# Kernel tuning notes

Hardware: AMD Instinct MI355X
Metric: run time of the kernel (lower is better)

Reference implementation:

```python
import jax, jax.numpy as jnp
import numpy as np

NUM_HEADS = 16
NUM_KV_HEADS = 4
ROPE_BASE = 10000.0
TRAIN_SEQ_LEN = 1024


def _rms_norm(x):
    eps = jnp.finfo(x.dtype).eps
    var = jnp.mean(jnp.square(x), axis=-1, keepdims=True)
    return x * jax.lax.rsqrt(var + eps)


def _rotary_cos_sin(seq_len, head_dim, dtype):
    # NTK-by-parts base scaling when seq_len > train_seq_len (matches Rotary.forward)
    if seq_len > TRAIN_SEQ_LEN:
        scale = seq_len / TRAIN_SEQ_LEN
        base = ROPE_BASE * scale ** (head_dim / (head_dim - 2))
    else:
        base = ROPE_BASE
    inv_freq = 1.0 / base ** (jnp.arange(0, head_dim, 2, dtype=jnp.float32) / head_dim)
    t = jnp.arange(seq_len, dtype=jnp.float32)
    freqs = jnp.outer(t, inv_freq)  # [S, head_dim//2]
    return jnp.cos(freqs).astype(dtype), jnp.sin(freqs).astype(dtype)


def _apply_rotary(x, cos, sin):
    # x: [B,S,H,D]; cos/sin: [S, D//2] broadcast over batch and heads
    half = x.shape[-1] // 2
    x1, x2 = x[..., :half], x[..., half:]
    c = cos[None, :, None, :]
    s = sin[None, :, None, :]
    return jnp.concatenate((x1 * c + x2 * s, -x1 * s + x2 * c), axis=-1)


def setup_inputs() -> dict:
    key = jax.random.key(0)
    ks = jax.random.split(key, 5)
    B, S, D = 2, 2048, 2048
    KVD = NUM_KV_HEADS * (D // NUM_HEADS)
    x = jax.random.normal(ks[0], (B, S, D), dtype=jnp.float32)
    Wq = jax.random.normal(ks[1], (D, D), dtype=jnp.float32) * 0.02
    Wk = jax.random.normal(ks[2], (KVD, D), dtype=jnp.float32) * 0.02
    Wv = jax.random.normal(ks[3], (KVD, D), dtype=jnp.float32) * 0.02
    Wproj = jax.random.normal(ks[4], (D, D), dtype=jnp.float32) * 0.02
    q_gain = jnp.ones((NUM_HEADS,), dtype=jnp.float32)
    return {"x": x, "Wq": Wq, "Wk": Wk, "Wv": Wv, "Wproj": Wproj, "q_gain": q_gain}


def reference(x, Wq, Wk, Wv, Wproj, q_gain):
    B, S, D = x.shape
    H, KH = NUM_HEADS, NUM_KV_HEADS
    hd = D // H
    group = H // KH

    q = (x @ Wq.T).reshape(B, S, H, hd)
    k = (x @ Wk.T).reshape(B, S, KH, hd)
    v = (x @ Wv.T).reshape(B, S, KH, hd)

    q = _rms_norm(q)
    k = _rms_norm(k)

    cos, sin = _rotary_cos_sin(S, hd, q.dtype)
    q = _apply_rotary(q, cos, sin)
    k = _apply_rotary(k, cos, sin)

    q = q * q_gain.astype(q.dtype)[None, None, :, None]

    # GQA: query head h attends to kv head h // group
    k = jnp.repeat(k, group, axis=2)  # [B,S,H,hd]
    v = jnp.repeat(v, group, axis=2)

    scale = 1.0 / jnp.sqrt(jnp.asarray(hd, dtype=q.dtype))
    scores = jnp.einsum("bshd,bthd->bhst", q, k) * scale  # [B,H,S,S]
    causal = jnp.tril(jnp.ones((S, S), dtype=bool))
    scores = jnp.where(causal[None, None], scores, jnp.asarray(-jnp.inf, scores.dtype))
    probs = jax.nn.softmax(scores, axis=-1)
    out = jnp.einsum("bhst,bthd->bshd", probs, v)  # [B,S,H,hd]

    return out.reshape(B, S, D) @ Wproj.T
```

## Files before the change

### kernel.cpp

```cpp
#include <hip/hip_runtime.h>
#include <cmath>

typedef unsigned short u16;
typedef short v8s __attribute__((ext_vector_type(8)));
typedef float v4f __attribute__((ext_vector_type(4)));
typedef unsigned short v4u __attribute__((ext_vector_type(4)));
typedef unsigned int v2u __attribute__((ext_vector_type(2)));

__device__ __forceinline__ u16 f2bf(float f) {
  unsigned u = __builtin_bit_cast(unsigned, f);
  u += 0x7fffu + ((u >> 16) & 1u);
  return (u16)(u >> 16);
}
__device__ __forceinline__ float bf2f(u16 h) {
  unsigned u = ((unsigned)h) << 16;
  return __builtin_bit_cast(float, u);
}
__device__ __forceinline__ unsigned pk2(float a, float b) {
  return (unsigned)f2bf(a) | ((unsigned)f2bf(b) << 16);
}

__global__ void k_cast_bf16(const float* __restrict__ in, u16* __restrict__ out, int n4) {
  int i = blockIdx.x * blockDim.x + threadIdx.x;
  if (i >= n4) return;
  v4f v = ((const v4f*)in)[i];
  v4u o;
  o[0] = f2bf(v[0]); o[1] = f2bf(v[1]); o[2] = f2bf(v[2]); o[3] = f2bf(v[3]);
  ((v4u*)out)[i] = o;
}

__global__ void k_cast_w(const float* __restrict__ a, const float* __restrict__ b,
                         const float* __restrict__ c, const float* __restrict__ d,
                         u16* __restrict__ oa, u16* __restrict__ ob, u16* __restrict__ oc,
                         u16* __restrict__ od, int na4, int nb4, int nc4, int nd4) {
  int j = blockIdx.x * blockDim.x + threadIdx.x;
  const float* src;
  u16* dst;
  if (j < na4) { src = a; dst = oa; }
  else {
    j -= na4;
    if (j < nb4) { src = b; dst = ob; }
    else {
      j -= nb4;
      if (j < nc4) { src = c; dst = oc; }
      else {
        j -= nc4;
        if (j >= nd4) return;
        src = d; dst = od;
      }
    }
  }
  v4f v = ((const v4f*)src)[j];
  v4u o;
  o[0] = f2bf(v[0]); o[1] = f2bf(v[1]); o[2] = f2bf(v[2]); o[3] = f2bf(v[3]);
  ((v4u*)dst)[j] = o;
}

__global__ void k_rope_tab(float* __restrict__ cosT, float* __restrict__ sinT, float log2_base) {
  int idx = blockIdx.x * blockDim.x + threadIdx.x;
  int t = idx >> 6, i = idx & 63;
  float inv = exp2f(-(float)i * (1.0f / 64.0f) * log2_base);
  float fr = (float)t * inv;
  cosT[idx] = cosf(fr);
  sinT[idx] = sinf(fr);
}

__global__ void k_rmsnorm_rope(u16* __restrict__ qk, const float* __restrict__ cosT,
                               const float* __restrict__ sinT, const float* __restrict__ gain,
                               int H, int S, float oscale) {
  int row = blockIdx.x * 4 + (threadIdx.x >> 6);
  int l = threadIdx.x & 63;
  int h = row % H;
  int m = row / H;
  int s = m % S;
  u16* p = qk + (size_t)row * 128;
  float a = bf2f(p[l]), b = bf2f(p[64 + l]);
  float ss = a * a + b * b;
#pragma unroll
  for (int o = 32; o; o >>= 1) ss += __shfl_xor(ss, o, 64);
  float r = rsqrtf(ss * (1.0f / 128.0f) + 1.1920929e-7f);
  a *= r; b *= r;
  float c = cosT[s * 64 + l], sn = sinT[s * 64 + l];
  float o1 = a * c + b * sn;
  float o2 = b * c - a * sn;
  float g = oscale;
  if (gain != nullptr) g *= gain[h];
  p[l] = f2bf(o1 * g);
  p[64 + l] = f2bf(o2 * g);
}

__device__ __forceinline__ void stage8(char* sL, const u16* __restrict__ Ag,
                                       const u16* __restrict__ Bg, int row0, int col0, int K,
                                       int n, int NT2, int tid) {
  int tile = n >> 2;
  if (tile >= NT2) return;
  int part = n & 3;
  int isB = (part & 1);
  int half = (part == 1 || part == 2) ? 1 : 0;
  const u16* src0 = isB ? Bg : Ag;
  int g0 = (isB ? col0 : row0) + half * 128;
  int k0 = tile * 64;
  char* base = sL + ((tile & 1) * 65536 + isB * 32768 + half * 16384);
#pragma unroll
  for (int j = 0; j < 2; ++j) {
    int o = (j * 512 + tid) * 16;
    int rowp = o >> 8;
    int off = o & 255;
    int un = off ^ ((rowp & 15) << 4);
    int rsub = rowp + ((un >> 7) << 6);
    int k = (un & 127) >> 1;
    const u16* src = src0 + (size_t)(g0 + rsub) * K + (k0 + k);
    __builtin_amdgcn_global_load_lds((const __attribute__((address_space(1))) void*)src,
                                     (__attribute__((address_space(3))) void*)(base + o), 16, 0, 0);
  }
}

#define PH(BUF, MH, NH, LA, LB, WAITC)                                                            \
  {                                                                                               \
    if (LA) {                                                                                     \
      _Pragma("unroll") for (int mi = 0; mi < 4; ++mi) {                                          \
        _Pragma("unroll") for (int c = 0; c < 2; ++c) {                                           \
          af[mi][c] = *(const v8s*)(sL + (BUF)*65536 + (MH)*16384 + (mi * 16 + lr) * 256 +        \
                                    ((wm * 128 + c * 64 + lh * 16) ^ (lr << 4)));                 \
        }                                                                                         \
      }                                                                                           \
    }                                                                                             \
    if (LB) {                                                                                     \
      _Pragma("unroll") for (int ni = 0; ni < 2; ++ni) {                                          \
        _Pragma("unroll") for (int c = 0; c < 2; ++c) {                                           \
          bf[ni][c] = *(const v8s*)(sL + (BUF)*65536 + 32768 + (NH)*16384 +                       \
                                    ((wn & 1) * 32 + ni * 16 + lr) * 256 +                        \
                                    (((wn >> 1) * 128 + c * 64 + lh * 16) ^ (lr << 4)));          \
        }                                                                                         \
      }                                                                                           \
    }                                                                                             \
    stage8(sL, Ag, Bg, row0, col0, K, n, NT2, tid);                                               \
    ++n;                                                                                          \
    if (WAITC) {                                                                                  \
      if (((n - 1) >> 2) < NT2) asm volatile("s_waitcnt vmcnt(4)" ::: "memory");                  \
      else asm volatile("s_waitcnt vmcnt(0)" ::: "memory");                                       \
    }                                                                                             \
    __builtin_amdgcn_sched_barrier(0);                                                            \
    __builtin_amdgcn_s_barrier();                                                                 \
    asm volatile("s_waitcnt lgkmcnt(0)" ::: "memory");                                            \
    __builtin_amdgcn_sched_barrier(0);                                                            \
    __builtin_amdgcn_s_setprio(1);                                                                \
    _Pragma("unroll") for (int mi = 0; mi < 4; ++mi) {                                            \
      _Pragma("unroll") for (int ni = 0; ni < 2; ++ni) {                                          \
        _Pragma("unroll") for (int c = 0; c < 2; ++c) {                                           \
          acc[(MH)*4 + mi][(NH)*2 + ni] = __builtin_amdgcn_mfma_f32_16x16x32_bf16(                \
              af[mi][c], bf[ni][c], acc[(MH)*4 + mi][(NH)*2 + ni], 0, 0, 0);                      \
        }                                                                                         \
      }                                                                                           \
    }                                                                                             \
    __builtin_amdgcn_s_setprio(0);                                                                \
    __builtin_amdgcn_sched_barrier(0);                                                            \
    __builtin_amdgcn_s_barrier();                                                                 \
  }

__global__ __launch_bounds__(512, 2) void k_gemm_qkv8(const u16* __restrict__ Ag,
                                                      const u16* __restrict__ Bg,
                                                      u16* __restrict__ q_o, u16* __restrict__ k_o,
                                                      u16* __restrict__ v_o, int M, int K) {
  __shared__ char sL[131072];
  const int tid = threadIdx.x;
  const int wid = tid >> 6, l = tid & 63;
  const int lr = l & 15, lh = l >> 4;
  const int wm = wid >> 2, wn = wid & 3;
  const int nwg = gridDim.x * gridDim.y;
  const int bid = blockIdx.y * gridDim.x + blockIdx.x;
  const int cpx = nwg >> 3;
  const int swz = (bid & 7) * cpx + (bid >> 3);
  const int row0 = (swz / gridDim.x) * 256, col0 = (swz % gridDim.x) * 256;
  const int NT2 = K >> 6;

  v4f zz = {0.f, 0.f, 0.f, 0.f};
  v4f acc[8][4];
#pragma unroll
  for (int i = 0; i < 8; ++i)
#pragma unroll
    for (int j = 0; j < 4; ++j) acc[i][j] = zz;
  v8s af[4][2], bf[2][2];

  for (int i = 0; i < 6; ++i) stage8(sL, Ag, Bg, row0, col0, K, i, NT2, tid);
  asm volatile("s_waitcnt vmcnt(4)" ::: "memory");
  __builtin_amdgcn_sched_barrier(0);
  __builtin_amdgcn_s_barrier();

  int n = 6;
  for (int it = 0; it < NT2 / 2; ++it) {
    PH(0, 0, 0, 1, 1, 0)
    PH(0, 0, 1, 0, 1, 0)
    PH(0, 1, 1, 1, 0, 0)
    PH(0, 1, 0, 0, 1, 1)
    PH(1, 0, 0, 1, 1, 0)
    PH(1, 0, 1, 0, 1, 0)
    PH(1, 1, 1, 1, 0, 0)
    PH(1, 1, 0, 0, 1, 1)
  }

  u16* outp;
  int ldo = 0, cb;
  bool tr = false;
  if (col0 < 2048) { outp = q_o; ldo = 2048; cb = col0; }
  else if (col0 < 2560) { outp = k_o; ldo = 512; cb = col0 - 2048; }
  else { outp = v_o; tr = true; cb = col0 - 2560; }
#pragma unroll
  for (int MH = 0; MH < 2; ++MH) {
#pragma unroll
    for (int mi = 0; mi < 4; ++mi) {
#pragma unroll
      for (int NH = 0; NH < 2; ++NH) {
#pragma unroll
        for (int ni = 0; ni < 2; ++ni) {
          int row = row0 + MH * 128 + wm * 64 + mi * 16 + lh * 4;
          int col = cb + NH * 128 + wn * 32 + ni * 16 + lr;
          v4f a_ = acc[MH * 4 + mi][NH * 2 + ni];
#pragma unroll
          for (int r = 0; r < 4; ++r) {
            u16 bv = f2bf(a_[r]);
            if (tr) outp[(size_t)col * M + row + r] = bv;
            else    outp[(size_t)(row + r) * ldo + col] = bv;
          }
        }
      }
    }
  }
}

__global__ __launch_bounds__(256) void k_gemm_bt(const u16* __restrict__ A,
                                                 const u16* __restrict__ Bw,
                                                 float* __restrict__ C, int M, int N, int K) {
  __shared__ u16 sA[128 * 32];
  __shared__ u16 sB[128 * 32];
  const int tid = threadIdx.x;
  const int w = tid >> 6, l = tid & 63;
  const int lr = l & 15, lh = l >> 4;
  const int wr = w >> 1, wc = w & 1;
  const int nwg = gridDim.x * gridDim.y;
  const int bid = blockIdx.y * gridDim.x + blockIdx.x;
  const int cpx = nwg >> 3;
  const int swz = (bid & 7) * cpx + (bid >> 3);
  const int row0 = (swz / gridDim.x) * 128, col0 = (swz % gridDim.x) * 128;
  v4f zz = {0.f, 0.f, 0.f, 0.f};
  v4f acc[4][4];
#pragma unroll
  for (int mi = 0; mi < 4; ++mi)
#pragma unroll
    for (int ni = 0; ni < 4; ++ni) acc[mi][ni] = zz;

  const int lrow = l >> 2;
  const int lcol = (l & 3) * 8;

  for (int k0 = 0; k0 < K; k0 += 32) {
#pragma unroll
    for (int i = 0; i < 2; ++i) {
      int c = i * 4 + w;
      const u16* srcA = A + (size_t)(row0 + c * 16 + lrow) * K + (k0 + lcol);
      const u16* srcB = Bw + (size_t)(col0 + c * 16 + lrow) * K + (k0 + lcol);
      __builtin_amdgcn_global_load_lds((const __attribute__((address_space(1))) void*)srcA,
                                       (__attribute__((address_space(3))) void*)(sA + c * 512),
                                       16, 0, 0);
      __builtin_amdgcn_global_load_lds((const __attribute__((address_space(1))) void*)srcB,
                                       (__attribute__((address_space(3))) void*)(sB + c * 512),
                                       16, 0, 0);
    }
    __syncthreads();
    v8s af[4], bfr[4];
#pragma unroll
    for (int mi = 0; mi < 4; ++mi)
      af[mi] = *(const v8s*)(sA + (wr * 64 + mi * 16 + lr) * 32 + lh * 8);
#pragma unroll
    for (int ni = 0; ni < 4; ++ni)
      bfr[ni] = *(const v8s*)(sB + (wc * 64 + ni * 16 + lr) * 32 + lh * 8);
#pragma unroll
    for (int mi = 0; mi < 4; ++mi)
#pragma unroll
      for (int ni = 0; ni < 4; ++ni)
        acc[mi][ni] = __builtin_amdgcn_mfma_f32_16x16x32_bf16(af[mi], bfr[ni], acc[mi][ni], 0, 0, 0);
    __syncthreads();
  }
#pragma unroll
  for (int mi = 0; mi < 4; ++mi) {
#pragma unroll
    for (int ni = 0; ni < 4; ++ni) {
      int row = row0 + wr * 64 + mi * 16 + lh * 4;
      int col = col0 + wc * 64 + ni * 16 + lr;
#pragma unroll
      for (int r = 0; r < 4; ++r) C[(size_t)(row + r) * N + col] = acc[mi][ni][r];
    }
  }
}

__global__ __launch_bounds__(256) void k_flash_attn(const u16* __restrict__ Q,
                                                    const u16* __restrict__ Kb,
                                                    const u16* __restrict__ Vt,
                                                    u16* __restrict__ O, int S, int H, int KH,
                                                    int Mtot) {
  const int bh = blockIdx.x;
  const int h = bh % H, b = bh / H;
  const int kvh = h / (H / KH);
  const int w = threadIdx.x >> 6, l = threadIdx.x & 63;
  const int lr = l & 15, lh = l >> 4;

  __shared__ alignas(16) char sK[2][16384];
  __shared__ alignas(16) char sV[2][16384];
  __shared__ alignas(16) unsigned P_lds[4][16 * 32];
  unsigned* prow = P_lds[w] + lr * 32;
  const int xr = (lr & 7) << 2;

  v4f zz = {0.f, 0.f, 0.f, 0.f};
  const int strideK = KH * 128;
  const int strideKB = strideK * 2;
  const char* KheadB = (const char*)Kb + 2 * ((size_t)b * S * strideK + (size_t)kvh * 128);
  const char* VheadB = (const char*)Vt + 2 * ((size_t)(kvh * 128) * Mtot + (size_t)b * S);
  const size_t MtotB = (size_t)Mtot * 2;

  auto stage = [&](int kv0, int bufi) {
    const char* Kt = KheadB + (size_t)kv0 * strideKB;
#pragma unroll
    for (int j = 0; j < 4; ++j) {
      int jj = w * 4 + j;
      int ci = jj * 64 + l;
      int r = ci >> 4;
      int bc = (ci & 15) << 4;
      const char* src = Kt + (size_t)r * strideKB + (bc ^ ((r & 15) << 4));
      __builtin_amdgcn_global_load_lds((const __attribute__((address_space(1))) void*)src,
                                       (__attribute__((address_space(3))) void*)(sK[bufi] + jj * 1024),
                                       16, 0, 0);
    }
    const char* Vt0 = VheadB + (size_t)kv0 * 2;
#pragma unroll
    for (int j = 0; j < 4; ++j) {
      int jj = w * 4 + j;
      int ci = jj * 64 + l;
      int r = ci >> 3;
      int bc = (ci & 7) << 4;
      const char* src = Vt0 + (size_t)r * MtotB + (bc ^ ((r & 7) << 4));
      __builtin_amdgcn_global_load_lds((const __attribute__((address_space(1))) void*)src,
                                       (__attribute__((address_space(3))) void*)(sV[bufi] + jj * 1024),
                                       16, 0, 0);
    }
  };

  for (int pp = 0; pp < 2; ++pp) {
    const int qt = (pp == 0) ? (int)blockIdx.y : (S / 64 - 1 - (int)blockIdx.y);
    const int q0 = qt * 64;
    const int nt = qt + 1;
    const int qi = q0 + w * 16 + lr;

    v8s qf[4];
    const u16* qp = Q + (size_t)(b * S + q0 + w * 16 + lr) * (size_t)(H * 128) + h * 128 + lh * 8;
#pragma unroll
    for (int c = 0; c < 4; ++c) qf[c] = *(const v8s*)(qp + c * 32);

    v4f o_acc[8];
#pragma unroll
    for (int df = 0; df < 8; ++df) o_acc[df] = zz;
    float m_run = -1e30f, l_run = 0.f;

    stage(0, 0);
    __syncthreads();

    int buf = 0;
    for (int t = 0; t < nt; ++t) {
      const int kv0 = t * 64;
      const bool lastTile = (t == nt - 1);
      const char* sKb = sK[buf];
      const char* sVb = sV[buf];

      v4f sv[4];
      __builtin_amdgcn_s_setprio(1);
#pragma unroll
      for (int nf = 0; nf < 4; ++nf) {
        v4f a_ = zz;
        const int r = nf * 16 + lr;
#pragma unroll
        for (int c = 0; c < 4; ++c) {
          v8s kf = *(const v8s*)(sKb + r * 256 + ((lh * 16 + c * 64) ^ (lr << 4)));
          a_ = __builtin_amdgcn_mfma_f32_16x16x32_bf16(kf, qf[c], a_, 0, 0, 0);
        }
        sv[nf] = a_;
      }
      __builtin_amdgcn_s_setprio(0);

      if (t + 1 < nt) stage(kv0 + 64, buf ^ 1);

      if (lastTile) {
#pragma unroll
        for (int nf = 0; nf < 4; ++nf)
#pragma unroll
          for (int r = 0; r < 4; ++r)
            if (kv0 + nf * 16 + lh * 4 + r > qi) sv[nf][r] = -1e30f;
      }
      float pmax = -1e30f;
#pragma unroll
      for (int nf = 0; nf < 4; ++nf)
#pragma unroll
        for (int r = 0; r < 4; ++r) pmax = fmaxf(pmax, sv[nf][r]);
      pmax = fmaxf(pmax, __shfl_xor(pmax, 16, 64));
      pmax = fmaxf(pmax, __shfl_xor(pmax, 32, 64));
      if (!__all(pmax - m_run <= 8.0f)) {
        float mnew = fmaxf(m_run, pmax);
        float corr = exp2f(m_run - mnew);
        l_run *= corr;
        m_run = mnew;
        float corrq[4];
#pragma unroll
        for (int r = 0; r < 4; ++r) corrq[r] = __shfl(corr, lh * 4 + r, 16);
#pragma unroll
        for (int df = 0; df < 8; ++df)
#pragma unroll
          for (int r = 0; r < 4; ++r) o_acc[df][r] *= corrq[r];
      }
      float rsum = 0.f;
#pragma unroll
      for (int nf = 0; nf < 4; ++nf)
#pragma unroll
        for (int r = 0; r < 4; ++r) {
          float pv = exp2f(sv[nf][r] - m_run);
          sv[nf][r] = pv;
          rsum += pv;
        }
      rsum += __shfl_xor(rsum, 16, 64);
      rsum += __shfl_xor(rsum, 32, 64);
      l_run += rsum;

#pragma unroll
      for (int nf = 0; nf < 4; ++nf) {
        v2u pw;
        pw[0] = pk2(sv[nf][0], sv[nf][1]);
        pw[1] = pk2(sv[nf][2], sv[nf][3]);
        *(v2u*)(prow + ((nf * 8 + lh * 2) ^ xr)) = pw;
      }
      asm volatile("s_waitcnt lgkmcnt(0)" ::: "memory");
      __builtin_amdgcn_sched_barrier(0);
      v8s ap[2];
#pragma unroll
      for (int c2 = 0; c2 < 2; ++c2) ap[c2] = *(const v8s*)(prow + ((c2 * 16 + lh * 4) ^ xr));

      __builtin_amdgcn_s_setprio(1);
#pragma unroll
      for (int df = 0; df < 8; ++df) {
        const int r = df * 16 + lr;
        const char* vrow = sVb + r * 128;
        const int key = (lr & 7) << 4;
#pragma unroll
        for (int c2 = 0; c2 < 2; ++c2) {
          v8s vf = *(const v8s*)(vrow + ((lh * 16 + c2 * 64) ^ key));
          o_acc[df] = __builtin_amdgcn_mfma_f32_16x16x32_bf16(ap[c2], vf, o_acc[df], 0, 0, 0);
        }
      }
      __builtin_amdgcn_s_setprio(0);

      __syncthreads();
      buf ^= 1;
    }

    float rl = 1.0f / l_run;
    float invq[4];
#pragma unroll
    for (int r = 0; r < 4; ++r) invq[r] = __shfl(rl, lh * 4 + r, 16);
    u16* op = O + (size_t)(b * S + q0 + w * 16 + lh * 4) * (size_t)(H * 128) + h * 128;
#pragma unroll
    for (int r = 0; r < 4; ++r)
#pragma unroll
      for (int df = 0; df < 8; ++df)
        op[(size_t)r * (H * 128) + df * 16 + lr] = f2bf(o_acc[df][r] * invq[r]);
  }
}

extern "C" void kernel_launch(void* const* d_in, const int* in_sizes, int n_in, void* d_out,
                              int out_size, void* d_ws, size_t ws_size, hipStream_t stream) {
  const float* x = (const float*)d_in[0];
  const float* Wq = (const float*)d_in[1];
  const float* Wk = (const float*)d_in[2];
  const float* Wv = (const float*)d_in[3];
  const float* Wp = (const float*)d_in[4];
  const float* gain = (const float*)d_in[5];
  float* out = (float*)d_out;

  const int B = 2, S = 2048, D = 2048, H = 16, KH = 4;
  const int M = B * S;
  const int KVD = KH * 128;
  const int NQKV = D + 2 * KVD;

  char* w = (char*)d_ws;
  u16* x_bf = (u16*)w;   w += (size_t)M * D * 2;
  u16* wqkv = (u16*)w;   w += (size_t)NQKV * D * 2;
  u16* wp_bf = (u16*)w;  w += (size_t)D * D * 2;
  u16* q_bf = (u16*)w;   w += (size_t)M * D * 2;
  u16* k_bf = (u16*)w;   w += (size_t)M * KVD * 2;
  u16* v_t = (u16*)w;    w += (size_t)M * KVD * 2;
  u16* ao_bf = (u16*)w;  w += (size_t)M * D * 2;
  float* cosT = (float*)w; w += (size_t)S * 64 * 4;
  float* sinT = (float*)w; w += (size_t)S * 64 * 4;
  if ((size_t)(w - (char*)d_ws) > ws_size) return;

  k_cast_bf16<<<(M * D / 4 + 255) / 256, 256, 0, stream>>>(x, x_bf, M * D / 4);
  {
    int na4 = D * D / 4, nb4 = KVD * D / 4, nc4 = KVD * D / 4, nd4 = D * D / 4;
    int tot = na4 + nb4 + nc4 + nd4;
    k_cast_w<<<(tot + 255) / 256, 256, 0, stream>>>(
        Wq, Wk, Wv, Wp, wqkv, wqkv + (size_t)D * D, wqkv + (size_t)(D + KVD) * D, wp_bf,
        na4, nb4, nc4, nd4);
  }

  double scale = (double)S / 1024.0;
  double base = (S > 1024) ? 10000.0 * pow(scale, 128.0 / 126.0) : 10000.0;
  float l2b = (float)(log(base) / log(2.0));
  k_rope_tab<<<S * 64 / 256, 256, 0, stream>>>(cosT, sinT, l2b);

  dim3 gqkv(NQKV / 256, M / 256);
  k_gemm_qkv8<<<gqkv, 512, 0, stream>>>(x_bf, wqkv, q_bf, k_bf, v_t, M, D);

  float qscale = 1.4426950408889634f / sqrtf(128.0f);
  k_rmsnorm_rope<<<(M * H) / 4, 256, 0, stream>>>(q_bf, cosT, sinT, gain, H, S, qscale);
  k_rmsnorm_rope<<<(M * KH) / 4, 256, 0, stream>>>(k_bf, cosT, sinT, nullptr, KH, S, 1.0f);

  dim3 blk(256);
  dim3 ga(B * H, S / 128);
  k_flash_attn<<<ga, blk, 0, stream>>>(q_bf, k_bf, v_t, ao_bf, S, H, KH, M);

  dim3 gp(D / 128, M / 128);
  k_gemm_bt<<<gp, blk, 0, stream>>>(ao_bf, wp_bf, out, M, D, D);
}
```

Baseline: 250.3 us.

## Reshape QKV GEMM block tile from 256x256 to 128x384

Changes the fused QKV projection GEMM block tile from 256x256 to 128 rows by 384 columns. The grid grows from 192 to 256 workgroups, which should fill more of the compute units. To fit the new shape, the LDS staging is rewritten so the A operand takes one load per thread and the B operand takes three, and the fragment loads and MFMA loops become 2x3 per wave. Because 2048 is not a multiple of 384, the epilogue now decides per column whether to write Q, K or transposed V. The cost is lower arithmetic reuse per block and uneven load counts per stage under the unchanged vmcnt waits.

```diff
diff --git a/kernel.cpp b/kernel.cpp
--- a/kernel.cpp
+++ b/kernel.cpp
@@ -95,41 +95,51 @@
   int tile = n >> 2;
   if (tile >= NT2) return;
   int part = n & 3;
-  int isB = (part & 1);
+  int isB = part & 1;
   int half = (part == 1 || part == 2) ? 1 : 0;
-  const u16* src0 = isB ? Bg : Ag;
-  int g0 = (isB ? col0 : row0) + half * 128;
   int k0 = tile * 64;
-  char* base = sL + ((tile & 1) * 65536 + isB * 32768 + half * 16384);
-#pragma unroll
-  for (int j = 0; j < 2; ++j) {
-    int o = (j * 512 + tid) * 16;
+  if (!isB) {
+    char* base = sL + (tile & 1) * 65536 + half * 8192;
+    int o = tid * 16;
     int rowp = o >> 8;
-    int off = o & 255;
-    int un = off ^ ((rowp & 15) << 4);
-    int rsub = rowp + ((un >> 7) << 6);
+    int un = (o & 255) ^ ((rowp & 15) << 4);
+    int rsub = rowp + ((un >> 7) << 5);
     int k = (un & 127) >> 1;
-    const u16* src = src0 + (size_t)(g0 + rsub) * K + (k0 + k);
+    const u16* src = Ag + (size_t)(row0 + half * 64 + rsub) * K + (k0 + k);
     __builtin_amdgcn_global_load_lds((const __attribute__((address_space(1))) void*)src,
                                      (__attribute__((address_space(3))) void*)(base + o), 16, 0, 0);
+  } else {
+    char* base = sL + (tile & 1) * 65536 + 16384 + half * 24576;
+#pragma unroll
+    for (int j = 0; j < 3; ++j) {
+      int o = (j * 512 + tid) * 16;
+      int rowp = o >> 8;
+      int un = (o & 255) ^ ((rowp & 15) << 4);
+      int rsub = rowp + (un >> 7) * 96;
+      int k = (un & 127) >> 1;
+      const u16* src = Bg + (size_t)(col0 + half * 192 + rsub) * K + (k0 + k);
+      __builtin_amdgcn_global_load_lds((const __attribute__((address_space(1))) void*)src,
+                                       (__attribute__((address_space(3))) void*)(base + o), 16, 0,
+                                       0);
+    }
   }
 }
 
 #define PH(BUF, MH, NH, LA, LB, WAITC)                                                            \
   {                                                                                               \
     if (LA) {                                                                                     \
-      _Pragma("unroll") for (int mi = 0; mi < 4; ++mi) {                                          \
+      _Pragma("unroll") for (int mi = 0; mi < 2; ++mi) {                                          \
         _Pragma("unroll") for (int c = 0; c < 2; ++c) {                                           \
-          af[mi][c] = *(const v8s*)(sL + (BUF)*65536 + (MH)*16384 + (mi * 16 + lr) * 256 +        \
+          af[mi][c] = *(const v8s*)(sL + (BUF)*65536 + (MH)*8192 + (mi * 16 + lr) * 256 +         \
                                     ((wm * 128 + c * 64 + lh * 16) ^ (lr << 4)));                 \
         }                                                                                         \
       }                                                                                           \
     }                                                                                             \
     if (LB) {                                                                                     \
-      _Pragma("unroll") for (int ni = 0; ni < 2; ++ni) {                                          \
+      _Pragma("unroll") for (int ni = 0; ni < 3; ++ni) {                                          \
         _Pragma("unroll") for (int c = 0; c < 2; ++c) {                                           \
-          bf[ni][c] = *(const v8s*)(sL + (BUF)*65536 + 32768 + (NH)*16384 +                       \
-                                    ((wn & 1) * 32 + ni * 16 + lr) * 256 +                        \
+          bf[ni][c] = *(const v8s*)(sL + (BUF)*65536 + 16384 + (NH)*24576 +                       \
+                                    ((wn & 1) * 48 + ni * 16 + lr) * 256 +                        \
                                     (((wn >> 1) * 128 + c * 64 + lh * 16) ^ (lr << 4)));          \
         }                                                                                         \
       }                                                                                           \
@@ -145,11 +155,11 @@
     asm volatile("s_waitcnt lgkmcnt(0)" ::: "memory");                                            \
     __builtin_amdgcn_sched_barrier(0);                                                            \
     __builtin_amdgcn_s_setprio(1);                                                                \
-    _Pragma("unroll") for (int mi = 0; mi < 4; ++mi) {                                            \
-      _Pragma("unroll") for (int ni = 0; ni < 2; ++ni) {                                          \
+    _Pragma("unroll") for (int mi = 0; mi < 2; ++mi) {                                            \
+      _Pragma("unroll") for (int ni = 0; ni < 3; ++ni) {                                          \
         _Pragma("unroll") for (int c = 0; c < 2; ++c) {                                           \
-          acc[(MH)*4 + mi][(NH)*2 + ni] = __builtin_amdgcn_mfma_f32_16x16x32_bf16(                \
-              af[mi][c], bf[ni][c], acc[(MH)*4 + mi][(NH)*2 + ni], 0, 0, 0);                      \
+          acc[(MH)*2 + mi][(NH)*3 + ni] = __builtin_amdgcn_mfma_f32_16x16x32_bf16(                \
+              af[mi][c], bf[ni][c], acc[(MH)*2 + mi][(NH)*3 + ni], 0, 0, 0);                      \
         }                                                                                         \
       }                                                                                           \
     }                                                                                             \
@@ -171,16 +181,16 @@
   const int bid = blockIdx.y * gridDim.x + blockIdx.x;
   const int cpx = nwg >> 3;
   const int swz = (bid & 7) * cpx + (bid >> 3);
-  const int row0 = (swz / gridDim.x) * 256, col0 = (swz % gridDim.x) * 256;
+  const int row0 = (swz / gridDim.x) * 128, col0 = (swz % gridDim.x) * 384;
   const int NT2 = K >> 6;
 
   v4f zz = {0.f, 0.f, 0.f, 0.f};
-  v4f acc[8][4];
-#pragma unroll
-  for (int i = 0; i < 8; ++i)
-#pragma unroll
-    for (int j = 0; j < 4; ++j) acc[i][j] = zz;
-  v8s af[4][2], bf[2][2];
+  v4f acc[4][6];
+#pragma unroll
+  for (int i = 0; i < 4; ++i)
+#pragma unroll
+    for (int j = 0; j < 6; ++j) acc[i][j] = zz;
+  v8s af[2][2], bf[3][2];
 
   for (int i = 0; i < 6; ++i) stage8(sL, Ag, Bg, row0, col0, K, i, NT2, tid);
   asm volatile("s_waitcnt vmcnt(4)" ::: "memory");
@@ -199,28 +209,26 @@
     PH(1, 1, 0, 0, 1, 1)
   }
 
-  u16* outp;
-  int ldo = 0, cb;
-  bool tr = false;
-  if (col0 < 2048) { outp = q_o; ldo = 2048; cb = col0; }
-  else if (col0 < 2560) { outp = k_o; ldo = 512; cb = col0 - 2048; }
-  else { outp = v_o; tr = true; cb = col0 - 2560; }
 #pragma unroll
   for (int MH = 0; MH < 2; ++MH) {
 #pragma unroll
-    for (int mi = 0; mi < 4; ++mi) {
+    for (int mi = 0; mi < 2; ++mi) {
 #pragma unroll
       for (int NH = 0; NH < 2; ++NH) {
 #pragma unroll
-        for (int ni = 0; ni < 2; ++ni) {
-          int row = row0 + MH * 128 + wm * 64 + mi * 16 + lh * 4;
-          int col = cb + NH * 128 + wn * 32 + ni * 16 + lr;
-          v4f a_ = acc[MH * 4 + mi][NH * 2 + ni];
-#pragma unroll
-          for (int r = 0; r < 4; ++r) {
-            u16 bv = f2bf(a_[r]);
-            if (tr) outp[(size_t)col * M + row + r] = bv;
-            else    outp[(size_t)(row + r) * ldo + col] = bv;
+        for (int ni = 0; ni < 3; ++ni) {
+          int row = row0 + MH * 64 + wm * 32 + mi * 16 + lh * 4;
+          int col = col0 + NH * 192 + wn * 48 + ni * 16 + lr;
+          v4f a_ = acc[MH * 2 + mi][NH * 3 + ni];
+          if (col < 2048) {
+#pragma unroll
+            for (int r = 0; r < 4; ++r) q_o[(size_t)(row + r) * 2048 + col] = f2bf(a_[r]);
+          } else if (col < 2560) {
+#pragma unroll
+            for (int r = 0; r < 4; ++r) k_o[(size_t)(row + r) * 512 + (col - 2048)] = f2bf(a_[r]);
+          } else {
+#pragma unroll
+            for (int r = 0; r < 4; ++r) v_o[(size_t)(col - 2560) * M + row + r] = f2bf(a_[r]);
           }
         }
       }
@@ -511,7 +519,7 @@
   float l2b = (float)(log(base) / log(2.0));
   k_rope_tab<<<S * 64 / 256, 256, 0, stream>>>(cosT, sinT, l2b);
 
-  dim3 gqkv(NQKV / 256, M / 256);
+  dim3 gqkv(NQKV / 384, M / 128);
   k_gemm_qkv8<<<gqkv, 512, 0, stream>>>(x_bf, wqkv, q_bf, k_bf, v_t, M, D);
 
   float qscale = 1.4426950408889634f / sqrtf(128.0f);
```

Result: faster. 225.1 us (-10.1%).
